# Kernel optimization log

Hardware: AMD Instinct MI355X
Metric: run time of the kernel (lower is better)

Reference implementation:

```python
import jax, jax.numpy as jnp
import numpy as np

B, N, IN_DIM, OUT_DIM, HEADS = 32, 10, 65536, 64, 8
D = OUT_DIM // HEADS  # = 8; torch.matmul only typechecks because D == HEADS


def setup_inputs() -> dict:
    key = jax.random.key(0)
    k1, k2, k3 = jax.random.split(key, 3)
    x = jax.random.normal(k1, (B, N, IN_DIM), dtype=jnp.float32)
    adj = jax.random.uniform(k2, (B, N, N), dtype=jnp.float32)
    # nn.Linear(in_dim, out_dim, bias=False) weight has shape (out_dim, in_dim)
    W = jax.random.normal(k3, (OUT_DIM, IN_DIM), dtype=jnp.float32) / np.float32(np.sqrt(IN_DIM))
    return {"x": x, "adj": adj, "W": W}


def reference(x, adj, W):
    b, n, _ = x.shape
    # W(x): (B, N, out_dim) -> view (B, N, heads, D)
    xt = (x @ W.T).reshape(b, n, HEADS, D)
    # torch.matmul(x_transformed, adj_expanded) with adj_expanded[b,n,k,m] = adj[b,n,m]
    # => result[b,n,h,m] = sum_k xt[b,n,h,k] * adj[b,n,m]
    result = jnp.einsum('bnhk,bnm->bnhm', xt, adj)
    result = result.reshape(32, 10, -1)  # hardcoded in the original module
    return jax.nn.relu(result)
```

## Files before the change

### kernel.cpp

```cpp
#include <hip/hip_runtime.h>
#include <hip/hip_bf16.h>

#define BB 32
#define NN 10
#define IN_DIM 65536
#define HEADS 8
#define DD 8
#define ROWS (BB*NN)
#define MTILES (ROWS/16)
#define KGRPS 1024
#define KB_PER_GRP 2
#define KFLOATS (KB_PER_GRP*32)
#define PAIRS (ROWS*HEADS)

typedef __attribute__((ext_vector_type(8))) short bf16x8;
typedef __attribute__((ext_vector_type(4))) float f32x4;

static __device__ __forceinline__ short f2bf(float f) {
    __hip_bfloat16 h = __float2bfloat16(f);
    return *reinterpret_cast<short*>(&h);
}

__global__ __launch_bounds__(256, 4) void gemv_fused_kernel(const float* __restrict__ x,
                                                            const float* __restrict__ W,
                                                            float* __restrict__ partials) {
    const int kgrp = blockIdx.x;
    const int t    = threadIdx.x;
    const int lane = t & 63;
    const int wave = t >> 6;

    __shared__ bf16x8 lds_b[KB_PER_GRP][64];

    if (wave < KB_PER_GRP) {
        const int kbl  = wave;
        const int head = lane & 15;
        const int kq   = lane >> 4;
        bf16x8 o = {0,0,0,0,0,0,0,0};
        if (head < HEADS) {
            float s0=0,s1=0,s2=0,s3=0,s4=0,s5=0,s6=0,s7=0;
            const float* wbase = W + (size_t)(head * DD) * IN_DIM
                               + kgrp * KFLOATS + kbl * 32 + kq * 8;
#pragma unroll
            for (int d = 0; d < DD; ++d) {
                const float4* p = (const float4*)(wbase + (size_t)d * IN_DIM);
                float4 lo = p[0], hi = p[1];
                s0 += lo.x; s1 += lo.y; s2 += lo.z; s3 += lo.w;
                s4 += hi.x; s5 += hi.y; s6 += hi.z; s7 += hi.w;
            }
            o[0]=f2bf(s0); o[1]=f2bf(s1); o[2]=f2bf(s2); o[3]=f2bf(s3);
            o[4]=f2bf(s4); o[5]=f2bf(s5); o[6]=f2bf(s6); o[7]=f2bf(s7);
        }
        lds_b[kbl][lane] = o;
    }
    __syncthreads();

    const bf16x8 b0 = lds_b[0][lane];
    const bf16x8 b1 = lds_b[1][lane];

    const int kq   = lane >> 4;
    const int head = lane & 15;
    const int r0   = (lane >> 4) * 4;
    const size_t xoff = (size_t)kgrp * KFLOATS + kq * 8;
    float* pbase = partials + (size_t)kgrp * PAIRS;

#pragma unroll
    for (int m = 0; m < MTILES / 4; ++m) {
        const int mtile = wave * (MTILES / 4) + m;
        const int row   = mtile * 16 + (lane & 15);
        const float* xr = x + (size_t)row * IN_DIM + xoff;

        f32x4 acc = {0.f, 0.f, 0.f, 0.f};
        {
            const float4* p = (const float4*)(xr + 0 * 32);
            float4 lo = p[0], hi = p[1];
            bf16x8 a;
            a[0]=f2bf(lo.x); a[1]=f2bf(lo.y); a[2]=f2bf(lo.z); a[3]=f2bf(lo.w);
            a[4]=f2bf(hi.x); a[5]=f2bf(hi.y); a[6]=f2bf(hi.z); a[7]=f2bf(hi.w);
            acc = __builtin_amdgcn_mfma_f32_16x16x32_bf16(a, b0, acc, 0, 0, 0);
        }
        {
            const float4* p = (const float4*)(xr + 1 * 32);
            float4 lo = p[0], hi = p[1];
            bf16x8 a;
            a[0]=f2bf(lo.x); a[1]=f2bf(lo.y); a[2]=f2bf(lo.z); a[3]=f2bf(lo.w);
            a[4]=f2bf(hi.x); a[5]=f2bf(hi.y); a[6]=f2bf(hi.z); a[7]=f2bf(hi.w);
            acc = __builtin_amdgcn_mfma_f32_16x16x32_bf16(a, b1, acc, 0, 0, 0);
        }

        if (head < HEADS) {
#pragma unroll
            for (int j = 0; j < 4; ++j)
                pbase[(size_t)(mtile * 16 + r0 + j) * HEADS + head] = acc[j];
        }
    }
}

__global__ __launch_bounds__(256) void finalize_kernel(const float* __restrict__ partials,
                                                       const float* __restrict__ adj,
                                                       float* __restrict__ out) {
    const int b  = blockIdx.x;
    const int t  = threadIdx.x;
    const int pr = t & 15;
    const int gs = t >> 4;
    const int pair = b * 16 + pr;

    float s = 0.f;
    const float* p = partials + (size_t)gs * 64 * PAIRS + pair;
#pragma unroll 8
    for (int g = 0; g < 64; ++g)
        s += p[(size_t)g * PAIRS];

    __shared__ float red[16][16];
    red[gs][pr] = s;
    __syncthreads();

    if (t < 16) {
        float tot = 0.f;
#pragma unroll
        for (int i = 0; i < 16; ++i) tot += red[i][t];
        const int pair2 = b * 16 + t;
        const int bn = pair2 >> 3;
        const int h  = pair2 & 7;
        const float* a = adj + bn * NN;
        float* o = out + bn * (HEADS * NN) + h * NN;
#pragma unroll
        for (int m = 0; m < NN; ++m) {
            float v = tot * a[m];
            o[m] = v > 0.f ? v : 0.f;
        }
    }
}

extern "C" void kernel_launch(void* const* d_in, const int* in_sizes, int n_in,
                              void* d_out, int out_size, void* d_ws, size_t ws_size,
                              hipStream_t stream) {
    const float* x   = (const float*)d_in[0];
    const float* adj = (const float*)d_in[1];
    const float* W   = (const float*)d_in[2];
    float* out = (float*)d_out;

    float* partials = (float*)d_ws;

    gemv_fused_kernel<<<KGRPS, 256, 0, stream>>>(x, W, partials);

    finalize_kernel<<<160, 256, 0, stream>>>(partials, adj, out);
}
```

Measured before the change: 27.81 us.

## Halve K-groups, store bf16 partials, and software-pipeline x loads across tiles

The GEMV kernel now handles twice as much K per block: 512 blocks, 4 k-blocks each, and all four waves build the W head-sums. Each wave processes 5 m-tiles with x loads issued ahead of the MFMA work, so several tiles' loads are in flight. Partials are stored as bf16 instead of fp32, and there are half as many of them, which cuts workspace write and read traffic in the finalize kernel. The cost is lower precision in the partial sums, higher register pressure (launch bounds drop to 2), and fewer blocks to spread over the CUs.

```diff
diff --git a/kernel.cpp b/kernel.cpp
--- a/kernel.cpp
+++ b/kernel.cpp
@@ -8,22 +8,49 @@
 #define DD 8
 #define ROWS (BB*NN)
 #define MTILES (ROWS/16)
-#define KGRPS 1024
-#define KB_PER_GRP 2
+#define KGRPS 512
+#define KB_PER_GRP 4
 #define KFLOATS (KB_PER_GRP*32)
 #define PAIRS (ROWS*HEADS)
 
 typedef __attribute__((ext_vector_type(8))) short bf16x8;
 typedef __attribute__((ext_vector_type(4))) float f32x4;
+typedef unsigned short u16;
 
 static __device__ __forceinline__ short f2bf(float f) {
     __hip_bfloat16 h = __float2bfloat16(f);
     return *reinterpret_cast<short*>(&h);
 }
-
-__global__ __launch_bounds__(256, 4) void gemv_fused_kernel(const float* __restrict__ x,
+static __device__ __forceinline__ u16 f2bfu(float f) {
+    __hip_bfloat16 h = __float2bfloat16(f);
+    return *reinterpret_cast<u16*>(&h);
+}
+static __device__ __forceinline__ float bf2f(u16 u) {
+    unsigned int v = ((unsigned int)u) << 16;
+    return *reinterpret_cast<float*>(&v);
+}
+
+struct XBuf { float4 a, b, c, d, e, f, g, h; };
+
+static __device__ __forceinline__ XBuf loadx(const float4* q) {
+    XBuf r;
+    r.a = q[0];  r.b = q[1];
+    r.c = q[8];  r.d = q[9];
+    r.e = q[16]; r.f = q[17];
+    r.g = q[24]; r.h = q[25];
+    return r;
+}
+
+static __device__ __forceinline__ bf16x8 cvt8(float4 lo, float4 hi) {
+    bf16x8 a;
+    a[0]=f2bf(lo.x); a[1]=f2bf(lo.y); a[2]=f2bf(lo.z); a[3]=f2bf(lo.w);
+    a[4]=f2bf(hi.x); a[5]=f2bf(hi.y); a[6]=f2bf(hi.z); a[7]=f2bf(hi.w);
+    return a;
+}
+
+__global__ __launch_bounds__(256, 2) void gemv_fused_kernel(const float* __restrict__ x,
                                                             const float* __restrict__ W,
-                                                            float* __restrict__ partials) {
+                                                            u16* __restrict__ partials) {
     const int kgrp = blockIdx.x;
     const int t    = threadIdx.x;
     const int lane = t & 63;
@@ -31,8 +58,8 @@
 
     __shared__ bf16x8 lds_b[KB_PER_GRP][64];
 
-    if (wave < KB_PER_GRP) {
-        const int kbl  = wave;
+    {
+        const int kbl  = t >> 6;
         const int head = lane & 15;
         const int kq   = lane >> 4;
         bf16x8 o = {0,0,0,0,0,0,0,0};
@@ -56,46 +83,83 @@
 
     const bf16x8 b0 = lds_b[0][lane];
     const bf16x8 b1 = lds_b[1][lane];
-
-    const int kq   = lane >> 4;
+    const bf16x8 b2 = lds_b[2][lane];
+    const bf16x8 b3 = lds_b[3][lane];
+
     const int head = lane & 15;
     const int r0   = (lane >> 4) * 4;
+    const int ln   = lane & 15;
+    const int kq   = lane >> 4;
     const size_t xoff = (size_t)kgrp * KFLOATS + kq * 8;
-    float* pbase = partials + (size_t)kgrp * PAIRS;
-
-#pragma unroll
-    for (int m = 0; m < MTILES / 4; ++m) {
-        const int mtile = wave * (MTILES / 4) + m;
-        const int row   = mtile * 16 + (lane & 15);
-        const float* xr = x + (size_t)row * IN_DIM + xoff;
-
-        f32x4 acc = {0.f, 0.f, 0.f, 0.f};
-        {
-            const float4* p = (const float4*)(xr + 0 * 32);
-            float4 lo = p[0], hi = p[1];
-            bf16x8 a;
-            a[0]=f2bf(lo.x); a[1]=f2bf(lo.y); a[2]=f2bf(lo.z); a[3]=f2bf(lo.w);
-            a[4]=f2bf(hi.x); a[5]=f2bf(hi.y); a[6]=f2bf(hi.z); a[7]=f2bf(hi.w);
-            acc = __builtin_amdgcn_mfma_f32_16x16x32_bf16(a, b0, acc, 0, 0, 0);
-        }
-        {
-            const float4* p = (const float4*)(xr + 1 * 32);
-            float4 lo = p[0], hi = p[1];
-            bf16x8 a;
-            a[0]=f2bf(lo.x); a[1]=f2bf(lo.y); a[2]=f2bf(lo.z); a[3]=f2bf(lo.w);
-            a[4]=f2bf(hi.x); a[5]=f2bf(hi.y); a[6]=f2bf(hi.z); a[7]=f2bf(hi.w);
-            acc = __builtin_amdgcn_mfma_f32_16x16x32_bf16(a, b1, acc, 0, 0, 0);
-        }
-
-        if (head < HEADS) {
-#pragma unroll
-            for (int j = 0; j < 4; ++j)
-                pbase[(size_t)(mtile * 16 + r0 + j) * HEADS + head] = acc[j];
-        }
-    }
-}
-
-__global__ __launch_bounds__(256) void finalize_kernel(const float* __restrict__ partials,
+    u16* pbase = partials + (size_t)kgrp * PAIRS;
+
+    const int mt0 = wave * 5;
+    const float4* q0 = (const float4*)(x + (size_t)((mt0+0)*16 + ln) * IN_DIM + xoff);
+    const float4* q1 = (const float4*)(x + (size_t)((mt0+1)*16 + ln) * IN_DIM + xoff);
+    const float4* q2 = (const float4*)(x + (size_t)((mt0+2)*16 + ln) * IN_DIM + xoff);
+    const float4* q3 = (const float4*)(x + (size_t)((mt0+3)*16 + ln) * IN_DIM + xoff);
+    const float4* q4 = (const float4*)(x + (size_t)((mt0+4)*16 + ln) * IN_DIM + xoff);
+
+    XBuf xb0 = loadx(q0);
+    XBuf xb1 = loadx(q1);
+
+    f32x4 acc;
+    XBuf xb2 = loadx(q2);
+    acc = (f32x4){0.f,0.f,0.f,0.f};
+    acc = __builtin_amdgcn_mfma_f32_16x16x32_bf16(cvt8(xb0.a, xb0.b), b0, acc, 0,0,0);
+    acc = __builtin_amdgcn_mfma_f32_16x16x32_bf16(cvt8(xb0.c, xb0.d), b1, acc, 0,0,0);
+    acc = __builtin_amdgcn_mfma_f32_16x16x32_bf16(cvt8(xb0.e, xb0.f), b2, acc, 0,0,0);
+    acc = __builtin_amdgcn_mfma_f32_16x16x32_bf16(cvt8(xb0.g, xb0.h), b3, acc, 0,0,0);
+    if (head < HEADS) {
+#pragma unroll
+        for (int j = 0; j < 4; ++j)
+            pbase[(size_t)((mt0+0)*16 + r0 + j) * HEADS + head] = f2bfu(acc[j]);
+    }
+    XBuf xb3 = loadx(q3);
+    acc = (f32x4){0.f,0.f,0.f,0.f};
+    acc = __builtin_amdgcn_mfma_f32_16x16x32_bf16(cvt8(xb1.a, xb1.b), b0, acc, 0,0,0);
+    acc = __builtin_amdgcn_mfma_f32_16x16x32_bf16(cvt8(xb1.c, xb1.d), b1, acc, 0,0,0);
+    acc = __builtin_amdgcn_mfma_f32_16x16x32_bf16(cvt8(xb1.e, xb1.f), b2, acc, 0,0,0);
+    acc = __builtin_amdgcn_mfma_f32_16x16x32_bf16(cvt8(xb1.g, xb1.h), b3, acc, 0,0,0);
+    if (head < HEADS) {
+#pragma unroll
+        for (int j = 0; j < 4; ++j)
+            pbase[(size_t)((mt0+1)*16 + r0 + j) * HEADS + head] = f2bfu(acc[j]);
+    }
+    XBuf xb4 = loadx(q4);
+    acc = (f32x4){0.f,0.f,0.f,0.f};
+    acc = __builtin_amdgcn_mfma_f32_16x16x32_bf16(cvt8(xb2.a, xb2.b), b0, acc, 0,0,0);
+    acc = __builtin_amdgcn_mfma_f32_16x16x32_bf16(cvt8(xb2.c, xb2.d), b1, acc, 0,0,0);
+    acc = __builtin_amdgcn_mfma_f32_16x16x32_bf16(cvt8(xb2.e, xb2.f), b2, acc, 0,0,0);
+    acc = __builtin_amdgcn_mfma_f32_16x16x32_bf16(cvt8(xb2.g, xb2.h), b3, acc, 0,0,0);
+    if (head < HEADS) {
+#pragma unroll
+        for (int j = 0; j < 4; ++j)
+            pbase[(size_t)((mt0+2)*16 + r0 + j) * HEADS + head] = f2bfu(acc[j]);
+    }
+    acc = (f32x4){0.f,0.f,0.f,0.f};
+    acc = __builtin_amdgcn_mfma_f32_16x16x32_bf16(cvt8(xb3.a, xb3.b), b0, acc, 0,0,0);
+    acc = __builtin_amdgcn_mfma_f32_16x16x32_bf16(cvt8(xb3.c, xb3.d), b1, acc, 0,0,0);
+    acc = __builtin_amdgcn_mfma_f32_16x16x32_bf16(cvt8(xb3.e, xb3.f), b2, acc, 0,0,0);
+    acc = __builtin_amdgcn_mfma_f32_16x16x32_bf16(cvt8(xb3.g, xb3.h), b3, acc, 0,0,0);
+    if (head < HEADS) {
+#pragma unroll
+        for (int j = 0; j < 4; ++j)
+            pbase[(size_t)((mt0+3)*16 + r0 + j) * HEADS + head] = f2bfu(acc[j]);
+    }
+    acc = (f32x4){0.f,0.f,0.f,0.f};
+    acc = __builtin_amdgcn_mfma_f32_16x16x32_bf16(cvt8(xb4.a, xb4.b), b0, acc, 0,0,0);
+    acc = __builtin_amdgcn_mfma_f32_16x16x32_bf16(cvt8(xb4.c, xb4.d), b1, acc, 0,0,0);
+    acc = __builtin_amdgcn_mfma_f32_16x16x32_bf16(cvt8(xb4.e, xb4.f), b2, acc, 0,0,0);
+    acc = __builtin_amdgcn_mfma_f32_16x16x32_bf16(cvt8(xb4.g, xb4.h), b3, acc, 0,0,0);
+    if (head < HEADS) {
+#pragma unroll
+        for (int j = 0; j < 4; ++j)
+            pbase[(size_t)((mt0+4)*16 + r0 + j) * HEADS + head] = f2bfu(acc[j]);
+    }
+}
+
+__global__ __launch_bounds__(256) void finalize_kernel(const u16* __restrict__ partials,
                                                        const float* __restrict__ adj,
                                                        float* __restrict__ out) {
     const int b  = blockIdx.x;
@@ -105,10 +169,10 @@
     const int pair = b * 16 + pr;
 
     float s = 0.f;
-    const float* p = partials + (size_t)gs * 64 * PAIRS + pair;
+    const u16* p = partials + (size_t)gs * 32 * PAIRS + pair;
 #pragma unroll 8
-    for (int g = 0; g < 64; ++g)
-        s += p[(size_t)g * PAIRS];
+    for (int g = 0; g < 32; ++g)
+        s += bf2f(p[(size_t)g * PAIRS]);
 
     __shared__ float red[16][16];
     red[gs][pr] = s;
@@ -139,7 +203,7 @@
     const float* W   = (const float*)d_in[2];
     float* out = (float*)d_out;
 
-    float* partials = (float*)d_ws;
+    u16* partials = (u16*)d_ws;
 
     gemv_fused_kernel<<<KGRPS, 256, 0, stream>>>(x, W, partials);
 
```

Result: faster. 26.03 us (-6.4%).

## Stage x tiles through LDS with register double buffering and halve K-groups

Applied to the files above, without the earlier changes.

The GEMV kernel now uses 512 blocks of 128 K-floats each instead of 1024 blocks of 64. Each thread issues coalesced row loads of x into registers, converts them to bf16, and stores them in a padded double-buffered LDS tile. MFMAs read their operands from LDS, and global loads for the next stage are overlapped with compute on the current one. This is meant to improve load coalescing and latency hiding and to halve the partials traffic in finalize, at the cost of more LDS use, extra barriers and lower occupancy.

```diff
diff --git a/kernel.cpp b/kernel.cpp
--- a/kernel.cpp
+++ b/kernel.cpp
@@ -1,27 +1,52 @@
 #include <hip/hip_runtime.h>
 #include <hip/hip_bf16.h>
 
-#define BB 32
 #define NN 10
 #define IN_DIM 65536
 #define HEADS 8
 #define DD 8
-#define ROWS (BB*NN)
-#define MTILES (ROWS/16)
-#define KGRPS 1024
-#define KB_PER_GRP 2
-#define KFLOATS (KB_PER_GRP*32)
+#define ROWS 320
+#define MTILES 20
+#define KGRPS 512
+#define KB_PER_GRP 4
+#define KFLOATS 128
 #define PAIRS (ROWS*HEADS)
+#define STAGES 5
+#define LROW 136
 
 typedef __attribute__((ext_vector_type(8))) short bf16x8;
 typedef __attribute__((ext_vector_type(4))) float f32x4;
+typedef unsigned short u16;
 
 static __device__ __forceinline__ short f2bf(float f) {
     __hip_bfloat16 h = __float2bfloat16(f);
     return *reinterpret_cast<short*>(&h);
 }
 
-__global__ __launch_bounds__(256, 4) void gemv_fused_kernel(const float* __restrict__ x,
+static __device__ __forceinline__ bf16x8 cvt8(float4 lo, float4 hi) {
+    bf16x8 a;
+    a[0]=f2bf(lo.x); a[1]=f2bf(lo.y); a[2]=f2bf(lo.z); a[3]=f2bf(lo.w);
+    a[4]=f2bf(hi.x); a[5]=f2bf(hi.y); a[6]=f2bf(hi.z); a[7]=f2bf(hi.w);
+    return a;
+}
+
+struct XR { float4 r0,r1,r2,r3,r4,r5,r6,r7; };
+
+static __device__ __forceinline__ void load_stage(XR& d, const float* __restrict__ x,
+                                                  int kgrp, int s, int t) {
+    const float4* src = (const float4*)(x + (size_t)(64*s + (t>>2)) * IN_DIM
+                                          + (size_t)kgrp * KFLOATS + (t&3)*32);
+    d.r0=src[0]; d.r1=src[1]; d.r2=src[2]; d.r3=src[3];
+    d.r4=src[4]; d.r5=src[5]; d.r6=src[6]; d.r7=src[7];
+}
+
+static __device__ __forceinline__ void write_stage(const XR& d, u16* dst) {
+    bf16x8* p = (bf16x8*)dst;
+    p[0]=cvt8(d.r0,d.r1); p[1]=cvt8(d.r2,d.r3);
+    p[2]=cvt8(d.r4,d.r5); p[3]=cvt8(d.r6,d.r7);
+}
+
+__global__ __launch_bounds__(256, 2) void gemv_fused_kernel(const float* __restrict__ x,
                                                             const float* __restrict__ W,
                                                             float* __restrict__ partials) {
     const int kgrp = blockIdx.x;
@@ -30,9 +55,13 @@
     const int wave = t >> 6;
 
     __shared__ bf16x8 lds_b[KB_PER_GRP][64];
+    __shared__ __align__(16) u16 xbuf[2][64][LROW];
 
-    if (wave < KB_PER_GRP) {
-        const int kbl  = wave;
+    XR A, B;
+    load_stage(A, x, kgrp, 0, t);
+
+    {
+        const int kbl  = t >> 6;
         const int head = lane & 15;
         const int kq   = lane >> 4;
         bf16x8 o = {0,0,0,0,0,0,0,0};
@@ -56,43 +85,62 @@
 
     const bf16x8 b0 = lds_b[0][lane];
     const bf16x8 b1 = lds_b[1][lane];
+    const bf16x8 b2 = lds_b[2][lane];
+    const bf16x8 b3 = lds_b[3][lane];
 
-    const int kq   = lane >> 4;
+    u16* wdst = &xbuf[0][0][0] + (size_t)(t >> 2) * LROW + (t & 3) * 32;
+    const size_t bufstride = (size_t)64 * LROW;
+
+    write_stage(A, wdst);
+    load_stage(B, x, kgrp, 1, t);
+    __syncthreads();
+
     const int head = lane & 15;
     const int r0   = (lane >> 4) * 4;
-    const size_t xoff = (size_t)kgrp * KFLOATS + kq * 8;
+    const int kq   = lane >> 4;
     float* pbase = partials + (size_t)kgrp * PAIRS;
+    const u16* rowp = &xbuf[0][0][0] + (size_t)(wave * 16 + (lane & 15)) * LROW + kq * 8;
 
-#pragma unroll
-    for (int m = 0; m < MTILES / 4; ++m) {
-        const int mtile = wave * (MTILES / 4) + m;
-        const int row   = mtile * 16 + (lane & 15);
-        const float* xr = x + (size_t)row * IN_DIM + xoff;
+#define COMPUTE_STAGE(BUFIDX, MT)                                              \
+    {                                                                          \
+        const bf16x8* q = (const bf16x8*)(rowp + (BUFIDX) * bufstride);        \
+        f32x4 acc = {0.f,0.f,0.f,0.f};                                         \
+        acc = __builtin_amdgcn_mfma_f32_16x16x32_bf16(q[0],  b0, acc, 0,0,0);  \
+        acc = __builtin_amdgcn_mfma_f32_16x16x32_bf16(q[4],  b1, acc, 0,0,0);  \
+        acc = __builtin_amdgcn_mfma_f32_16x16x32_bf16(q[8],  b2, acc, 0,0,0);  \
+        acc = __builtin_amdgcn_mfma_f32_16x16x32_bf16(q[12], b3, acc, 0,0,0);  \
+        if (head < HEADS) {                                                    \
+            _Pragma("unroll")                                                  \
+            for (int j = 0; j < 4; ++j)                                        \
+                pbase[(size_t)((MT)*16 + r0 + j) * HEADS + head] = acc[j];     \
+        }                                                                      \
+    }
 
-        f32x4 acc = {0.f, 0.f, 0.f, 0.f};
-        {
-            const float4* p = (const float4*)(xr + 0 * 32);
-            float4 lo = p[0], hi = p[1];
-            bf16x8 a;
-            a[0]=f2bf(lo.x); a[1]=f2bf(lo.y); a[2]=f2bf(lo.z); a[3]=f2bf(lo.w);
-            a[4]=f2bf(hi.x); a[5]=f2bf(hi.y); a[6]=f2bf(hi.z); a[7]=f2bf(hi.w);
-            acc = __builtin_amdgcn_mfma_f32_16x16x32_bf16(a, b0, acc, 0, 0, 0);
-        }
-        {
-            const float4* p = (const float4*)(xr + 1 * 32);
-            float4 lo = p[0], hi = p[1];
-            bf16x8 a;
-            a[0]=f2bf(lo.x); a[1]=f2bf(lo.y); a[2]=f2bf(lo.z); a[3]=f2bf(lo.w);
-            a[4]=f2bf(hi.x); a[5]=f2bf(hi.y); a[6]=f2bf(hi.z); a[7]=f2bf(hi.w);
-            acc = __builtin_amdgcn_mfma_f32_16x16x32_bf16(a, b1, acc, 0, 0, 0);
-        }
+    load_stage(A, x, kgrp, 2, t);
+    COMPUTE_STAGE(0, wave);
+    __syncthreads();
+    write_stage(B, wdst + bufstride);
+    __syncthreads();
 
-        if (head < HEADS) {
-#pragma unroll
-            for (int j = 0; j < 4; ++j)
-                pbase[(size_t)(mtile * 16 + r0 + j) * HEADS + head] = acc[j];
-        }
-    }
+    load_stage(B, x, kgrp, 3, t);
+    COMPUTE_STAGE(1, 4 + wave);
+    __syncthreads();
+    write_stage(A, wdst);
+    __syncthreads();
+
+    load_stage(A, x, kgrp, 4, t);
+    COMPUTE_STAGE(0, 8 + wave);
+    __syncthreads();
+    write_stage(B, wdst + bufstride);
+    __syncthreads();
+
+    COMPUTE_STAGE(1, 12 + wave);
+    __syncthreads();
+    write_stage(A, wdst);
+    __syncthreads();
+
+    COMPUTE_STAGE(0, 16 + wave);
+#undef COMPUTE_STAGE
 }
 
 __global__ __launch_bounds__(256) void finalize_kernel(const float* __restrict__ partials,
@@ -105,9 +153,9 @@
     const int pair = b * 16 + pr;
 
     float s = 0.f;
-    const float* p = partials + (size_t)gs * 64 * PAIRS + pair;
+    const float* p = partials + (size_t)gs * 32 * PAIRS + pair;
 #pragma unroll 8
-    for (int g = 0; g < 64; ++g)
+    for (int g = 0; g < 32; ++g)
         s += p[(size_t)g * PAIRS];
 
     __shared__ float red[16][16];
```

After: 27.00 us. -2.9%, faster.
